# Kernel tuning notes

Hardware: AMD Instinct MI355X
Metric: run time of the kernel (lower is better)

## Reference

```python
import jax, jax.numpy as jnp
import numpy as np

R, B, D = 1024, 16, 1024
K_ACTIVE = 20
FB_DECAY = 0.9          # feedback_decay
REFR_W = 1.0            # refractory_weight
FB_W = 0.5              # feedback_weight


def _hex_neighbors(rows=32, cols=32):
    """Toroidal hex grid adjacency: 6 neighbors per region, shape [R, 6]."""
    n = rows * cols
    idx = np.arange(n)
    r, c = idx // cols, idx % cols
    def wrap(rr, cc):
        return (rr % rows) * cols + (cc % cols)
    nbrs = np.stack([
        wrap(r, c - 1), wrap(r, c + 1),
        wrap(r - 1, c), wrap(r + 1, c),
        wrap(r - 1, c + 1), wrap(r + 1, c - 1),
    ], axis=1)
    return nbrs.astype(np.int32)


def setup_inputs() -> dict:
    key = jax.random.key(0)
    k1, k2, k3, k4, k5 = jax.random.split(key, 5)
    return {
        "H": jax.random.normal(k1, (R, B, D), jnp.float32),
        "neighbor_msg": jax.random.normal(k2, (R, B, D), jnp.float32),
        "w": jax.random.normal(k3, (D,), jnp.float32) / np.float32(np.sqrt(D)),
        "theta": jnp.zeros((R,), jnp.float32),
        "refractory": jax.random.uniform(k4, (B, R), jnp.float32),
        "feedback": jax.random.uniform(k5, (B, R), jnp.float32),
        "neighbor_indices": jnp.asarray(_hex_neighbors()),
    }


def _greedy_hex_nms(adj, nbrs, k):
    """adj: [B, R] adjusted scores; nbrs: [R, 6]. Returns hard mask [B, R]."""
    n_regions = adj.shape[1]

    def nms_one(scores):
        order = jnp.argsort(-scores)  # descending

        def step(state, idx):
            sel, sup, cnt = state
            take = (cnt < k) & (~sel[idx]) & (~sup[idx])
            sel = sel.at[idx].set(sel[idx] | take)
            sup = sup.at[idx].set(sup[idx] | take)
            nb = nbrs[idx]  # [6]
            sup = sup.at[nb].set(sup[nb] | take)
            return (sel, sup, cnt + take.astype(jnp.int32)), None

        init = (jnp.zeros(n_regions, bool), jnp.zeros(n_regions, bool), jnp.int32(0))
        (sel, _, _), _ = jax.lax.scan(step, init, order)
        return sel.astype(scores.dtype)

    return jax.vmap(nms_one)(adj)


def reference(H, neighbor_msg, w, theta, refractory, feedback, neighbor_indices):
    # learned score: Linear(D, 1, bias=False) -> [B, R]
    s = jnp.einsum('rbd,d->br', H, w)
    # feedback inhibition from routed message magnitude
    fb_mag = jnp.linalg.norm(neighbor_msg, axis=-1).T          # [B, R]
    fb_new = FB_DECAY * feedback + (1.0 - FB_DECAY) * fb_mag   # updated _feedback
    adj = s - theta[None, :] - REFR_W * refractory - FB_W * fb_new
    hard = jax.lax.stop_gradient(_greedy_hex_nms(adj, neighbor_indices, K_ACTIVE))
    soft = jax.nn.sigmoid(adj)
    ste = hard + soft - jax.lax.stop_gradient(soft)            # straight-through
    Hs = H * ste.T[:, :, None]                                 # [R, B, D]
    return Hs, hard, adj
```

## Files before the change

### kernel.cpp

```cpp
#include <hip/hip_runtime.h>
#include <math.h>

#define RR 1024
#define BB 16
#define DD 1024
#define K_ACTIVE 20

typedef float f32x4 __attribute__((ext_vector_type(4)));

__global__ __launch_bounds__(256, 4) void score_kernel(
    const float* __restrict__ H, const float* __restrict__ msg,
    const float* __restrict__ w, const float* __restrict__ theta,
    const float* __restrict__ refr, const float* __restrict__ fb,
    float* __restrict__ adj_out, float* __restrict__ Hs)
{
    const int wave = threadIdx.x >> 6;
    const int lane = threadIdx.x & 63;
    const int pair = blockIdx.x * 4 + wave;
    const int r = pair >> 4;
    const int b = pair & 15;

    const float4* H4 = (const float4*)(H + (size_t)pair * DD);
    const float4* M4 = (const float4*)(msg + (size_t)pair * DD);
    const float4* W4 = (const float4*)w;
    f32x4* Z4 = (f32x4*)(Hs + (size_t)pair * DD);

    const f32x4 zero4 = (f32x4){0.f, 0.f, 0.f, 0.f};
#pragma unroll
    for (int k = 0; k < 4; ++k)
        __builtin_nontemporal_store(zero4, &Z4[lane + 64 * k]);

    float4 h[4], m[4], ww[4];
#pragma unroll
    for (int k = 0; k < 4; ++k) {
        const int i = lane + 64 * k;
        h[k]  = H4[i];
        m[k]  = M4[i];
        ww[k] = W4[i];
    }

    float dot = 0.f, ss = 0.f;
#pragma unroll
    for (int k = 0; k < 4; ++k) {
        dot += h[k].x * ww[k].x + h[k].y * ww[k].y + h[k].z * ww[k].z + h[k].w * ww[k].w;
        ss  += m[k].x * m[k].x + m[k].y * m[k].y + m[k].z * m[k].z + m[k].w * m[k].w;
    }
#pragma unroll
    for (int off = 32; off > 0; off >>= 1) {
        dot += __shfl_down(dot, off);
        ss  += __shfl_down(ss, off);
    }
    if (lane == 0) {
        const float fb_mag = sqrtf(ss);
        const float fb_new = 0.9f * fb[b * RR + r] + 0.1f * fb_mag;
        const float a = dot - theta[r] - refr[b * RR + r] - 0.5f * fb_new;
        adj_out[b * RR + r] = a;
    }
}

__global__ __launch_bounds__(256) void nms_gate_kernel(
    const float* __restrict__ adj, const int* __restrict__ nbrs,
    const float* __restrict__ H,
    float* __restrict__ hard, float* __restrict__ Hs)
{
    __shared__ int nb_lds[RR * 6];
    __shared__ int sel_r[K_ACTIVE];
    __shared__ int nsel_lds;

    const int b = blockIdx.x;
    const int tid = threadIdx.x;
    const int lane = tid & 63;
    const int wave = tid >> 6;

    {
        const int4* nb4 = (const int4*)nbrs;
        int4* nl4 = (int4*)nb_lds;
#pragma unroll
        for (int j = 0; j < 6; ++j)
            nl4[tid + 256 * j] = nb4[tid + 256 * j];
    }
    __syncthreads();

    if (wave == 0) {
        float v[16];
#pragma unroll
        for (int j = 0; j < 16; ++j)
            v[j] = adj[b * RR + lane + 64 * j];

        unsigned int sel = 0u;
        unsigned int dead = 0u;
        int nsel = 0;

        for (int it = 0; it < K_ACTIVE; ++it) {
            float tv[16]; int ti[16];
#pragma unroll
            for (int j = 0; j < 16; ++j) {
                tv[j] = ((dead >> j) & 1u) ? -INFINITY : v[j];
                ti[j] = lane + 64 * j;
            }
#pragma unroll
            for (int s = 8; s >= 1; s >>= 1) {
#pragma unroll
                for (int j = 0; j < 8; ++j) {
                    if (j < s) {
                        if (tv[j + s] > tv[j]) { tv[j] = tv[j + s]; ti[j] = ti[j + s]; }
                    }
                }
            }
            float m = tv[0];
            int mi = ti[0];

#pragma unroll
            for (int off = 32; off > 0; off >>= 1) {
                const float ov = __shfl_xor(m, off);
                const int   oi = __shfl_xor(mi, off);
                if (ov > m || (ov == m && oi < mi)) { m = ov; mi = oi; }
            }

            if (m == -INFINITY) break;

            if (lane == 0) sel_r[nsel] = mi;
            nsel++;

            int sup[7];
            sup[0] = mi;
            const int base = mi * 6;
#pragma unroll
            for (int k = 0; k < 6; ++k) sup[k + 1] = nb_lds[base + k];

            sel |= ((mi & 63) == lane) ? (1u << (mi >> 6)) : 0u;
#pragma unroll
            for (int k = 0; k < 7; ++k)
                dead |= ((sup[k] & 63) == lane) ? (1u << (sup[k] >> 6)) : 0u;
        }

        if (lane == 0) nsel_lds = nsel;

#pragma unroll
        for (int j = 0; j < 16; ++j)
            hard[b * RR + lane + 64 * j] = ((sel >> j) & 1u) ? 1.0f : 0.0f;
    }
    __syncthreads();

    const int nsel = nsel_lds;
    for (int s = 0; s < nsel; ++s) {
        const int r = sel_r[s];
        const size_t off = ((size_t)r * BB + b) * DD;
        ((float4*)(Hs + off))[tid] = ((const float4*)(H + off))[tid];
    }
}

extern "C" void kernel_launch(void* const* d_in, const int* in_sizes, int n_in,
                              void* d_out, int out_size, void* d_ws, size_t ws_size,
                              hipStream_t stream) {
    const float* H     = (const float*)d_in[0];
    const float* msg   = (const float*)d_in[1];
    const float* w     = (const float*)d_in[2];
    const float* theta = (const float*)d_in[3];
    const float* refr  = (const float*)d_in[4];
    const float* fb    = (const float*)d_in[5];
    const int*   nbrs  = (const int*)d_in[6];

    float* out  = (float*)d_out;
    float* Hs   = out;
    float* hard = out + (size_t)RR * BB * DD;
    float* adj  = hard + (size_t)BB * RR;

    score_kernel<<<RR * BB / 4, 256, 0, stream>>>(H, msg, w, theta, refr, fb, adj, Hs);
    nms_gate_kernel<<<BB, 256, 0, stream>>>(adj, nbrs, H, hard, Hs);
}
```

Baseline: 203.1 us.

## Split gating into separate kernel; move Hs zero-fill out of score kernel

Removes the zero-fill of Hs from the score kernel, so that kernel only reads H and msg. The NMS kernel shrinks to a single wave. A new grid-strided gate kernel writes every Hs row, copying H for selected pairs and zeros otherwise. This adds a third kernel launch, and it may reduce write pressure overlapping the score kernel's reads. The gate kernel re-reads only the selected H rows and writes the full output, so total traffic stays roughly the same.

```diff
diff --git a/kernel.cpp b/kernel.cpp
--- a/kernel.cpp
+++ b/kernel.cpp
@@ -12,7 +12,7 @@
     const float* __restrict__ H, const float* __restrict__ msg,
     const float* __restrict__ w, const float* __restrict__ theta,
     const float* __restrict__ refr, const float* __restrict__ fb,
-    float* __restrict__ adj_out, float* __restrict__ Hs)
+    float* __restrict__ adj_out)
 {
     const int wave = threadIdx.x >> 6;
     const int lane = threadIdx.x & 63;
@@ -23,12 +23,6 @@
     const float4* H4 = (const float4*)(H + (size_t)pair * DD);
     const float4* M4 = (const float4*)(msg + (size_t)pair * DD);
     const float4* W4 = (const float4*)w;
-    f32x4* Z4 = (f32x4*)(Hs + (size_t)pair * DD);
-
-    const f32x4 zero4 = (f32x4){0.f, 0.f, 0.f, 0.f};
-#pragma unroll
-    for (int k = 0; k < 4; ++k)
-        __builtin_nontemporal_store(zero4, &Z4[lane + 64 * k]);
 
     float4 h[4], m[4], ww[4];
 #pragma unroll
@@ -58,95 +52,96 @@
     }
 }
 
-__global__ __launch_bounds__(256) void nms_gate_kernel(
+__global__ __launch_bounds__(64) void nms_kernel(
     const float* __restrict__ adj, const int* __restrict__ nbrs,
-    const float* __restrict__ H,
-    float* __restrict__ hard, float* __restrict__ Hs)
+    float* __restrict__ hard)
 {
     __shared__ int nb_lds[RR * 6];
-    __shared__ int sel_r[K_ACTIVE];
-    __shared__ int nsel_lds;
 
     const int b = blockIdx.x;
-    const int tid = threadIdx.x;
-    const int lane = tid & 63;
-    const int wave = tid >> 6;
+    const int lane = threadIdx.x;
 
     {
         const int4* nb4 = (const int4*)nbrs;
         int4* nl4 = (int4*)nb_lds;
 #pragma unroll
-        for (int j = 0; j < 6; ++j)
-            nl4[tid + 256 * j] = nb4[tid + 256 * j];
+        for (int j = 0; j < 24; ++j)
+            nl4[lane + 64 * j] = nb4[lane + 64 * j];
     }
+
+    float v[16];
+#pragma unroll
+    for (int j = 0; j < 16; ++j)
+        v[j] = adj[b * RR + lane + 64 * j];
+
     __syncthreads();
 
-    if (wave == 0) {
-        float v[16];
+    unsigned int sel = 0u;
+    unsigned int dead = 0u;
+
+    for (int it = 0; it < K_ACTIVE; ++it) {
+        float tv[16]; int ti[16];
 #pragma unroll
-        for (int j = 0; j < 16; ++j)
-            v[j] = adj[b * RR + lane + 64 * j];
-
-        unsigned int sel = 0u;
-        unsigned int dead = 0u;
-        int nsel = 0;
-
-        for (int it = 0; it < K_ACTIVE; ++it) {
-            float tv[16]; int ti[16];
+        for (int j = 0; j < 16; ++j) {
+            tv[j] = ((dead >> j) & 1u) ? -INFINITY : v[j];
+            ti[j] = lane + 64 * j;
+        }
 #pragma unroll
-            for (int j = 0; j < 16; ++j) {
-                tv[j] = ((dead >> j) & 1u) ? -INFINITY : v[j];
-                ti[j] = lane + 64 * j;
-            }
+        for (int s = 8; s >= 1; s >>= 1) {
 #pragma unroll
-            for (int s = 8; s >= 1; s >>= 1) {
-#pragma unroll
-                for (int j = 0; j < 8; ++j) {
-                    if (j < s) {
-                        if (tv[j + s] > tv[j]) { tv[j] = tv[j + s]; ti[j] = ti[j + s]; }
-                    }
+            for (int j = 0; j < 8; ++j) {
+                if (j < s) {
+                    if (tv[j + s] > tv[j]) { tv[j] = tv[j + s]; ti[j] = ti[j + s]; }
                 }
             }
-            float m = tv[0];
-            int mi = ti[0];
+        }
+        float m = tv[0];
+        int mi = ti[0];
 
 #pragma unroll
-            for (int off = 32; off > 0; off >>= 1) {
-                const float ov = __shfl_xor(m, off);
-                const int   oi = __shfl_xor(mi, off);
-                if (ov > m || (ov == m && oi < mi)) { m = ov; mi = oi; }
-            }
-
-            if (m == -INFINITY) break;
-
-            if (lane == 0) sel_r[nsel] = mi;
-            nsel++;
-
-            int sup[7];
-            sup[0] = mi;
-            const int base = mi * 6;
-#pragma unroll
-            for (int k = 0; k < 6; ++k) sup[k + 1] = nb_lds[base + k];
-
-            sel |= ((mi & 63) == lane) ? (1u << (mi >> 6)) : 0u;
-#pragma unroll
-            for (int k = 0; k < 7; ++k)
-                dead |= ((sup[k] & 63) == lane) ? (1u << (sup[k] >> 6)) : 0u;
+        for (int off = 32; off > 0; off >>= 1) {
+            const float ov = __shfl_xor(m, off);
+            const int   oi = __shfl_xor(mi, off);
+            if (ov > m || (ov == m && oi < mi)) { m = ov; mi = oi; }
         }
 
-        if (lane == 0) nsel_lds = nsel;
+        if (m == -INFINITY) break;
+
+        int sup[7];
+        sup[0] = mi;
+        const int base = mi * 6;
+#pragma unroll
+        for (int k = 0; k < 6; ++k) sup[k + 1] = nb_lds[base + k];
+
+        sel |= ((mi & 63) == lane) ? (1u << (mi >> 6)) : 0u;
+#pragma unroll
+        for (int k = 0; k < 7; ++k)
+            dead |= ((sup[k] & 63) == lane) ? (1u << (sup[k] >> 6)) : 0u;
+    }
 
 #pragma unroll
-        for (int j = 0; j < 16; ++j)
-            hard[b * RR + lane + 64 * j] = ((sel >> j) & 1u) ? 1.0f : 0.0f;
-    }
-    __syncthreads();
+    for (int j = 0; j < 16; ++j)
+        hard[b * RR + lane + 64 * j] = ((sel >> j) & 1u) ? 1.0f : 0.0f;
+}
 
-    const int nsel = nsel_lds;
-    for (int s = 0; s < nsel; ++s) {
-        const int r = sel_r[s];
-        const size_t off = ((size_t)r * BB + b) * DD;
-        ((float4*)(Hs + off))[tid] = ((const float4*)(H + off))[tid];
+__global__ __launch_bounds__(256) void gate_kernel(
+    const float* __restrict__ H, const float* __restrict__ hard,
+    float* __restrict__ Hs)
+{
+    const int tid = threadIdx.x;
+    const f32x4 zero4 = (f32x4){0.f, 0.f, 0.f, 0.f};
+    for (int pair = blockIdx.x; pair < RR * BB; pair += gridDim.x) {
+        const int r = pair >> 4;
+        const int b = pair & 15;
+        const float g = hard[b * RR + r];
+        f32x4* out4 = (f32x4*)(Hs + (size_t)pair * DD);
+        if (g != 0.0f) {
+            const float4* H4 = (const float4*)(H + (size_t)pair * DD);
+            const float4 t = H4[tid];
+            __builtin_nontemporal_store((f32x4){t.x, t.y, t.z, t.w}, &out4[tid]);
+        } else {
+            __builtin_nontemporal_store(zero4, &out4[tid]);
+        }
     }
 }
 
@@ -166,6 +161,7 @@
     float* hard = out + (size_t)RR * BB * DD;
     float* adj  = hard + (size_t)BB * RR;
 
-    score_kernel<<<RR * BB / 4, 256, 0, stream>>>(H, msg, w, theta, refr, fb, adj, Hs);
-    nms_gate_kernel<<<BB, 256, 0, stream>>>(adj, nbrs, H, hard, Hs);
+    score_kernel<<<RR * BB / 4, 256, 0, stream>>>(H, msg, w, theta, refr, fb, adj);
+    nms_kernel<<<BB, 64, 0, stream>>>(adj, nbrs, hard);
+    gate_kernel<<<2048, 256, 0, stream>>>(H, hard, Hs);
 }
```

Measured after the change: 198.7 us. -2.2%, faster.

## Split zero-fill into separate kernel and load score inputs via global_load_lds

Applied to the files above, without the earlier changes.

Moves zeroing of the gated output into its own grid-stride kernel, leaving the score kernel read-only. The score kernel now handles four (r,b) pairs per wave, loads H and the message rows straight into LDS with global_load_lds, and loads w once per block. The goal is to keep reads and writes from competing inside one kernel and to cut register pressure. It adds an extra kernel launch, and the separate zero-fill kernel can no longer overlap its writes with the score kernel's reads.

```diff
diff --git a/kernel.cpp b/kernel.cpp
--- a/kernel.cpp
+++ b/kernel.cpp
@@ -8,53 +8,75 @@
 
 typedef float f32x4 __attribute__((ext_vector_type(4)));
 
-__global__ __launch_bounds__(256, 4) void score_kernel(
+__global__ __launch_bounds__(256) void zero_fill_kernel(float* __restrict__ Hs)
+{
+    const f32x4 z = (f32x4){0.f, 0.f, 0.f, 0.f};
+    f32x4* p = (f32x4*)Hs;
+    const int n = RR * BB * DD / 4;
+    for (int i = blockIdx.x * 256 + threadIdx.x; i < n; i += gridDim.x * 256)
+        __builtin_nontemporal_store(z, &p[i]);
+}
+
+__global__ __launch_bounds__(256) void score_kernel(
     const float* __restrict__ H, const float* __restrict__ msg,
     const float* __restrict__ w, const float* __restrict__ theta,
     const float* __restrict__ refr, const float* __restrict__ fb,
-    float* __restrict__ adj_out, float* __restrict__ Hs)
+    float* __restrict__ adj_out)
 {
-    const int wave = threadIdx.x >> 6;
+    __shared__ float4 hbuf[4][256];
+    __shared__ float4 mbuf[4][256];
+
     const int lane = threadIdx.x & 63;
-    const int pair = blockIdx.x * 4 + wave;
-    const int r = pair >> 4;
-    const int b = pair & 15;
+    const int wv   = threadIdx.x >> 6;
 
-    const float4* H4 = (const float4*)(H + (size_t)pair * DD);
-    const float4* M4 = (const float4*)(msg + (size_t)pair * DD);
     const float4* W4 = (const float4*)w;
-    f32x4* Z4 = (f32x4*)(Hs + (size_t)pair * DD);
+    float4 ww[4];
+#pragma unroll
+    for (int k = 0; k < 4; ++k) ww[k] = W4[lane + 64 * k];
 
-    const f32x4 zero4 = (f32x4){0.f, 0.f, 0.f, 0.f};
+    for (int t = 0; t < 4; ++t) {
+        const int pair = blockIdx.x * 16 + t * 4 + wv;
+        const int r = pair >> 4, b = pair & 15;
+
+        const float4* Hp = (const float4*)(H   + (size_t)pair * DD);
+        const float4* Mp = (const float4*)(msg + (size_t)pair * DD);
+
 #pragma unroll
-    for (int k = 0; k < 4; ++k)
-        __builtin_nontemporal_store(zero4, &Z4[lane + 64 * k]);
+        for (int k = 0; k < 4; ++k) {
+            __builtin_amdgcn_global_load_lds(
+                (const __attribute__((address_space(1))) void*)(Hp + k * 64 + lane),
+                (__attribute__((address_space(3))) void*)(&hbuf[wv][k * 64]),
+                16, 0, 0);
+            __builtin_amdgcn_global_load_lds(
+                (const __attribute__((address_space(1))) void*)(Mp + k * 64 + lane),
+                (__attribute__((address_space(3))) void*)(&mbuf[wv][k * 64]),
+                16, 0, 0);
+        }
 
-    float4 h[4], m[4], ww[4];
+        const float th = theta[r];
+        const float rf = refr[b * RR + r];
+        const float f0 = fb[b * RR + r];
+
+        asm volatile("s_waitcnt vmcnt(0)" ::: "memory");
+        __builtin_amdgcn_sched_barrier(0);
+
+        float dot = 0.f, ss = 0.f;
 #pragma unroll
-    for (int k = 0; k < 4; ++k) {
-        const int i = lane + 64 * k;
-        h[k]  = H4[i];
-        m[k]  = M4[i];
-        ww[k] = W4[i];
-    }
-
-    float dot = 0.f, ss = 0.f;
+        for (int k = 0; k < 4; ++k) {
+            const float4 hv = hbuf[wv][lane + 64 * k];
+            const float4 mv = mbuf[wv][lane + 64 * k];
+            dot += hv.x * ww[k].x + hv.y * ww[k].y + hv.z * ww[k].z + hv.w * ww[k].w;
+            ss  += mv.x * mv.x + mv.y * mv.y + mv.z * mv.z + mv.w * mv.w;
+        }
 #pragma unroll
-    for (int k = 0; k < 4; ++k) {
-        dot += h[k].x * ww[k].x + h[k].y * ww[k].y + h[k].z * ww[k].z + h[k].w * ww[k].w;
-        ss  += m[k].x * m[k].x + m[k].y * m[k].y + m[k].z * m[k].z + m[k].w * m[k].w;
-    }
-#pragma unroll
-    for (int off = 32; off > 0; off >>= 1) {
-        dot += __shfl_down(dot, off);
-        ss  += __shfl_down(ss, off);
-    }
-    if (lane == 0) {
-        const float fb_mag = sqrtf(ss);
-        const float fb_new = 0.9f * fb[b * RR + r] + 0.1f * fb_mag;
-        const float a = dot - theta[r] - refr[b * RR + r] - 0.5f * fb_new;
-        adj_out[b * RR + r] = a;
+        for (int off = 32; off > 0; off >>= 1) {
+            dot += __shfl_down(dot, off);
+            ss  += __shfl_down(ss, off);
+        }
+        if (lane == 0) {
+            const float fbn = 0.9f * f0 + 0.1f * sqrtf(ss);
+            adj_out[b * RR + r] = dot - th - rf - 0.5f * fbn;
+        }
     }
 }
 
@@ -166,6 +188,7 @@
     float* hard = out + (size_t)RR * BB * DD;
     float* adj  = hard + (size_t)BB * RR;
 
-    score_kernel<<<RR * BB / 4, 256, 0, stream>>>(H, msg, w, theta, refr, fb, adj, Hs);
+    zero_fill_kernel<<<2048, 256, 0, stream>>>(Hs);
+    score_kernel<<<1024, 256, 0, stream>>>(H, msg, w, theta, refr, fb, adj);
     nms_gate_kernel<<<BB, 256, 0, stream>>>(adj, nbrs, H, hard, Hs);
 }
```

After: 206.5 us. No clear change (+1.6%).
